# Optimization experiments

Hardware: AMD Instinct MI355X
Metric: run time of the kernel (lower is better)

The kernel has to match this reference:

```python
import jax, jax.numpy as jnp
import numpy as np

N = 50000        # nodes
E = 800000       # edges
F_IN = 32        # float features (x also carries 1 trailing cell-id column)
CELL_DIM = 16
NUM_CELLS = 854
C = 64           # out_channels
H0, H1 = 2, 1    # heads schedule for num_layers=2 -> [2, 1]
D_IN = F_IN + CELL_DIM  # 48, GAT input dim after cell embedding concat
NEG_SLOPE = 0.2  # PyG GATConv default negative_slope


def setup_inputs() -> dict:
    key = jax.random.key(0)
    ks = jax.random.split(key, 14)
    base = jax.random.normal(ks[0], (N, F_IN), jnp.float32)
    cell_ids = jax.random.randint(ks[1], (N,), 0, NUM_CELLS)
    x = jnp.concatenate([base, cell_ids.astype(jnp.float32)[:, None]], axis=1)
    edge_index = jax.random.randint(ks[2], (2, E), 0, N, dtype=jnp.int32)
    s = lambda f: 1.0 / np.sqrt(f)
    emb = jax.random.normal(ks[3], (NUM_CELLS, CELL_DIM), jnp.float32)
    W0 = jax.random.normal(ks[4], (D_IN, H0 * C), jnp.float32) * s(D_IN)
    a_src0 = jax.random.normal(ks[5], (H0, C), jnp.float32) * s(C)
    a_dst0 = jax.random.normal(ks[6], (H0, C), jnp.float32) * s(C)
    b0 = jnp.zeros((C,), jnp.float32)
    ln_g = jnp.ones((C,), jnp.float32)
    ln_b = jnp.zeros((C,), jnp.float32)
    W1 = jax.random.normal(ks[7], (C, H1 * C), jnp.float32) * s(C)
    a_src1 = jax.random.normal(ks[8], (H1, C), jnp.float32) * s(C)
    a_dst1 = jax.random.normal(ks[9], (H1, C), jnp.float32) * s(C)
    b1 = jnp.zeros((C,), jnp.float32)
    return {"x": x, "edge_index": edge_index, "emb": emb,
            "W0": W0, "a_src0": a_src0, "a_dst0": a_dst0, "b0": b0,
            "ln_g": ln_g, "ln_b": ln_b,
            "W1": W1, "a_src1": a_src1, "a_dst1": a_dst1, "b1": b1}


def gat_layer(h_in, src, dst, W, a_src, a_dst, b, heads):
    # h_in: [N, D]; src/dst: [E'] (self-loops already appended)
    h = (h_in @ W).reshape(N, heads, C)                 # [N, H, C]
    alpha_s = jnp.einsum('nhc,hc->nh', h, a_src)        # [N, H]
    alpha_d = jnp.einsum('nhc,hc->nh', h, a_dst)
    e = jax.nn.leaky_relu(alpha_s[src] + alpha_d[dst], NEG_SLOPE)  # [E', H]
    # segment softmax over incoming edges of each dst node
    m = jax.ops.segment_max(e, dst, num_segments=N)     # [N, H]
    ex = jnp.exp(e - m[dst])
    denom = jax.ops.segment_sum(ex, dst, num_segments=N)
    alpha = ex / denom[dst]                             # [E', H]
    msg = h[src] * alpha[:, :, None]                    # [E', H, C]
    out = jax.ops.segment_sum(msg, dst, num_segments=N) # [N, H, C]
    return out.mean(axis=1) + b                         # concat=False -> mean over heads


def layer_norm(x, g, b):
    mu = x.mean(-1, keepdims=True)
    var = ((x - mu) ** 2).mean(-1, keepdims=True)
    return (x - mu) * jax.lax.rsqrt(var + 1e-5) * g + b


def reference(x, edge_index, emb, W0, a_src0, a_dst0, b0, ln_g, ln_b,
              W1, a_src1, a_dst1, b1):
    base = x[:, :-1]
    cell_ids = x[:, -1].astype(jnp.int32)
    h = jnp.concatenate([base, emb[cell_ids]], axis=1)  # [N, 48]
    # add self-loops (PyG GATConv default add_self_loops=True)
    loop = jnp.arange(N, dtype=edge_index.dtype)
    src = jnp.concatenate([edge_index[0], loop])
    dst = jnp.concatenate([edge_index[1], loop])
    h = gat_layer(h, src, dst, W0, a_src0, a_dst0, b0, H0)
    h = jax.nn.elu(layer_norm(h, ln_g, ln_b))           # dropout is identity at eval
    h = gat_layer(h, src, dst, W1, a_src1, a_dst1, b1, H1)
    return h
```

## Files before the change

### kernel.cpp

```cpp
#include <hip/hip_runtime.h>
#include <hip/hip_bf16.h>

#define N_NODES 50000
#define N_EDGES 800000
#define E_TOT 850000
#define F_IN 32
#define CELL_DIM 16
#define D_IN 48
#define X_STRIDE 33
#define NUM_CELLS 854
#define NEG_SLOPE 0.2f
#define SCAN_BLOCKS 49
#define NODE0_BLOCKS 512

typedef unsigned int uint;
typedef unsigned short ushort;

static __device__ __forceinline__ uint f2b(float f) {
  uint x = __float_as_uint(f);
  return (x + 0x7fffu + ((x >> 16) & 1u)) >> 16;
}
static __device__ __forceinline__ float b2f_lo(uint w) { return __uint_as_float(w << 16); }
static __device__ __forceinline__ float b2f_hi(uint w) { return __uint_as_float(w & 0xffff0000u); }
static __device__ __forceinline__ float lrelu(float e) { return e > 0.f ? e : NEG_SLOPE * e; }


__global__ __launch_bounds__(256) void k_hist(const int* __restrict__ ei, int* __restrict__ deg) {
  int e = blockIdx.x * 256 + threadIdx.x;
  if (e < N_EDGES) atomicAdd(&deg[ei[N_EDGES + e]], 1);
}

__global__ __launch_bounds__(1024) void k_scan1(const int* __restrict__ deg, int* __restrict__ off,
                                                int* __restrict__ bsum) {
  __shared__ int ws[16];
  int tid = threadIdx.x;
  int lane = tid & 63, wid = tid >> 6;
  int i = blockIdx.x * 1024 + tid;
  int v = (i < N_NODES) ? deg[i] + 1 : 0;
  int sc = v;
#pragma unroll
  for (int o = 1; o < 64; o <<= 1) {
    int t = __shfl_up(sc, o, 64);
    if (lane >= o) sc += t;
  }
  if (lane == 63) ws[wid] = sc;
  __syncthreads();
  if (tid < 16) {
    int w = ws[tid];
    int s = w;
#pragma unroll
    for (int o = 1; o < 16; o <<= 1) {
      int t = __shfl_up(s, o, 64);
      if (tid >= o) s += t;
    }
    ws[tid] = s - w;
  }
  __syncthreads();
  int excl = sc - v + ws[wid];
  if (i < N_NODES) off[i] = excl;
  if (tid == 1023) bsum[blockIdx.x] = excl + v;
}

__global__ __launch_bounds__(1024) void k_scan23(int* __restrict__ off, int* __restrict__ ofs,
                                                 const int* __restrict__ bsum) {
  __shared__ int carry_s;
  int tid = threadIdx.x;
  if (tid < 64) {
    int v = (tid < SCAN_BLOCKS) ? bsum[tid] : 0;
    int s = v;
#pragma unroll
    for (int o = 1; o < 64; o <<= 1) {
      int t = __shfl_up(s, o, 64);
      if (tid >= o) s += t;
    }
    if (tid == (int)blockIdx.x) carry_s = s - v;
  }
  __syncthreads();
  int carry = carry_s;
  int i = blockIdx.x * 1024 + tid;
  if (i < N_NODES) {
    int v = off[i] + carry;
    off[i] = v;
    ofs[i] = v;
  }
  if (i == 0) off[N_NODES] = E_TOT;
}

__global__ __launch_bounds__(256) void k_scatter(const int* __restrict__ ei, int* __restrict__ ofs,
                                                 const int* __restrict__ off,
                                                 const float2* __restrict__ as0v,
                                                 const float2* __restrict__ ad0v,
                                                 uint2* __restrict__ ew) {
  int t = blockIdx.x * 256 + threadIdx.x;
  if (t < N_EDGES) {
    int s = ei[t], d = ei[N_EDGES + t];
    float2 a_s = as0v[s], a_d = ad0v[d];
    float w0 = __expf(lrelu(a_s.x + a_d.x));
    float w1 = __expf(lrelu(a_s.y + a_d.y));
    int p = atomicAdd(&ofs[d], 1);
    ew[p] = make_uint2((uint)s, f2b(w0) | (f2b(w1) << 16));
  } else if (t < N_EDGES + N_NODES) {
    int n = t - N_EDGES;
    int slot = off[n + 1] - 1;
    float2 a_s = as0v[n], a_d = ad0v[n];
    float w0 = __expf(lrelu(a_s.x + a_d.x));
    float w1 = __expf(lrelu(a_s.y + a_d.y));
    ew[slot] = make_uint2((uint)n, f2b(w0) | (f2b(w1) << 16));
  }
}


__global__ __launch_bounds__(256, 4) void k_node0(const float* __restrict__ x,
                                                  const float* __restrict__ emb,
                                                  const float* __restrict__ W0,
                                                  const float* __restrict__ asrc,
                                                  const float* __restrict__ adst,
                                                  uint* __restrict__ h0p,
                                                  float2* __restrict__ as0,
                                                  float2* __restrict__ ad0) {
  __shared__ float hin_s[4][4][48];
  int tid = threadIdx.x;
  int lane = tid & 63, wid = tid >> 6;
  float2 w0r[D_IN];
#pragma unroll
  for (int k = 0; k < D_IN; ++k)
    w0r[k] = make_float2(W0[k * 128 + lane], W0[k * 128 + 64 + lane]);
  float a_s0 = asrc[lane], a_s1 = asrc[64 + lane];
  float a_d0 = adst[lane], a_d1 = adst[64 + lane];

  int gw = blockIdx.x * 4 + wid;
  for (int g = gw; g < N_NODES / 4; g += NODE0_BLOCKS * 4) {
    int nb = g * 4;
#pragma unroll
    for (int j = 0; j < 4; ++j) {
      int n = nb + j;
      float t = 0.f;
      if (lane < 33) t = x[n * X_STRIDE + lane];
      int cid = (int)__shfl(t, 32, 64);
      cid = cid < 0 ? 0 : (cid >= NUM_CELLS ? NUM_CELLS - 1 : cid);
      if (lane >= 32 && lane < 48) t = emb[cid * CELL_DIM + (lane - 32)];
      if (lane < 48) hin_s[wid][j][lane] = t;
    }
#pragma unroll
    for (int j = 0; j < 4; ++j) {
      int n = nb + j;
      const float4* hp = (const float4*)hin_s[wid][j];
      float acc0 = 0.f, acc1 = 0.f;
#pragma unroll
      for (int k4 = 0; k4 < 12; ++k4) {
        float4 h = hp[k4];
        acc0 = fmaf(h.x, w0r[4 * k4 + 0].x, acc0); acc1 = fmaf(h.x, w0r[4 * k4 + 0].y, acc1);
        acc0 = fmaf(h.y, w0r[4 * k4 + 1].x, acc0); acc1 = fmaf(h.y, w0r[4 * k4 + 1].y, acc1);
        acc0 = fmaf(h.z, w0r[4 * k4 + 2].x, acc0); acc1 = fmaf(h.z, w0r[4 * k4 + 2].y, acc1);
        acc0 = fmaf(h.w, w0r[4 * k4 + 3].x, acc0); acc1 = fmaf(h.w, w0r[4 * k4 + 3].y, acc1);
      }
      h0p[n * 64 + lane] = f2b(acc0) | (f2b(acc1) << 16);
      float sa0 = acc0 * a_s0, sa1 = acc1 * a_s1;
      float sd0 = acc0 * a_d0, sd1 = acc1 * a_d1;
#pragma unroll
      for (int o = 32; o >= 1; o >>= 1) {
        sa0 += __shfl_xor(sa0, o, 64);
        sa1 += __shfl_xor(sa1, o, 64);
        sd0 += __shfl_xor(sd0, o, 64);
        sd1 += __shfl_xor(sd1, o, 64);
      }
      if (lane == 0) {
        as0[n] = make_float2(sa0, sa1);
        ad0[n] = make_float2(sd0, sd1);
      }
    }
  }
}


__global__ __launch_bounds__(256) void k_agg0(const int* __restrict__ off,
                                              const uint2* __restrict__ ew,
                                              const uint* __restrict__ h0p,
                                              const float* __restrict__ b0,
                                              const float* __restrict__ lng,
                                              const float* __restrict__ lnb,
                                              const float* __restrict__ W1,
                                              const float* __restrict__ asrc1,
                                              const float* __restrict__ adst1,
                                              ushort* __restrict__ h1b,
                                              float* __restrict__ as1, float* __restrict__ ad1) {
  int n = blockIdx.x * 4 + (threadIdx.x >> 6);
  int lane = threadIdx.x & 63;
  float acc0 = 0.f, acc1 = 0.f, den0 = 0.f, den1 = 0.f;
  int i0 = off[n], i1 = off[n + 1];
  int i = i0;
  for (; i + 7 < i1; i += 8) {
    uint2 r[8];
    uint h[8];
#pragma unroll
    for (int j = 0; j < 8; ++j) r[j] = ew[i + j];
#pragma unroll
    for (int j = 0; j < 8; ++j) h[j] = h0p[r[j].x * 64 + lane];
#pragma unroll
    for (int j = 0; j < 8; ++j) {
      float w;
      w = b2f_lo(r[j].y); acc0 += w * b2f_lo(h[j]); den0 += w;
      w = b2f_hi(r[j].y); acc1 += w * b2f_hi(h[j]); den1 += w;
    }
  }
  for (; i + 3 < i1; i += 4) {
    uint2 r[4];
    uint h[4];
#pragma unroll
    for (int j = 0; j < 4; ++j) r[j] = ew[i + j];
#pragma unroll
    for (int j = 0; j < 4; ++j) h[j] = h0p[r[j].x * 64 + lane];
#pragma unroll
    for (int j = 0; j < 4; ++j) {
      float w;
      w = b2f_lo(r[j].y); acc0 += w * b2f_lo(h[j]); den0 += w;
      w = b2f_hi(r[j].y); acc1 += w * b2f_hi(h[j]); den1 += w;
    }
  }
  for (; i < i1; ++i) {
    uint2 r = ew[i];
    uint h = h0p[r.x * 64 + lane];
    float w;
    w = b2f_lo(r.y); acc0 += w * b2f_lo(h); den0 += w;
    w = b2f_hi(r.y); acc1 += w * b2f_hi(h); den1 += w;
  }
  float v = 0.5f * (acc0 / den0 + acc1 / den1) + b0[lane];
  float mu = v;
#pragma unroll
  for (int o = 32; o >= 1; o >>= 1) mu += __shfl_xor(mu, o, 64);
  mu *= (1.0f / 64.0f);
  float d = v - mu;
  float vr = d * d;
#pragma unroll
  for (int o = 32; o >= 1; o >>= 1) vr += __shfl_xor(vr, o, 64);
  vr *= (1.0f / 64.0f);
  float y = d * rsqrtf(vr + 1e-5f) * lng[lane] + lnb[lane];
  y = y > 0.f ? y : expm1f(y);
  float h1v = 0.f;
#pragma unroll
  for (int k = 0; k < 64; ++k) {
    float yk = __shfl(y, k, 64);
    h1v += yk * W1[k * 64 + lane];
  }
  h1b[n * 64 + lane] = (ushort)f2b(h1v);
  float sa = h1v * asrc1[lane];
  float sdv = h1v * adst1[lane];
#pragma unroll
  for (int o = 32; o >= 1; o >>= 1) {
    sa += __shfl_xor(sa, o, 64);
    sdv += __shfl_xor(sdv, o, 64);
  }
  if (lane == 0) {
    as1[n] = sa;
    ad1[n] = sdv;
  }
}


__global__ __launch_bounds__(256) void k_agg1(const int* __restrict__ off,
                                              const uint2* __restrict__ ew,
                                              const ushort* __restrict__ h1b,
                                              const float* __restrict__ as1,
                                              const float* __restrict__ ad1,
                                              const float* __restrict__ b1,
                                              float* __restrict__ out) {
  int n = blockIdx.x * 4 + (threadIdx.x >> 6);
  int lane = threadIdx.x & 63;
  float adv = ad1[n];
  float acc = 0.f, den = 0.f;
  int i0 = off[n], i1 = off[n + 1];
  int i = i0;
  for (; i + 7 < i1; i += 8) {
    uint s[8];
    float a[8];
    uint h[8];
#pragma unroll
    for (int j = 0; j < 8; ++j) s[j] = ew[i + j].x;
#pragma unroll
    for (int j = 0; j < 8; ++j) a[j] = as1[s[j]];
#pragma unroll
    for (int j = 0; j < 8; ++j) h[j] = h1b[s[j] * 64 + lane];
#pragma unroll
    for (int j = 0; j < 8; ++j) {
      float w = __expf(lrelu(a[j] + adv));
      acc += w * __uint_as_float(h[j] << 16);
      den += w;
    }
  }
  for (; i + 3 < i1; i += 4) {
    uint s[4];
    float a[4];
    uint h[4];
#pragma unroll
    for (int j = 0; j < 4; ++j) s[j] = ew[i + j].x;
#pragma unroll
    for (int j = 0; j < 4; ++j) a[j] = as1[s[j]];
#pragma unroll
    for (int j = 0; j < 4; ++j) h[j] = h1b[s[j] * 64 + lane];
#pragma unroll
    for (int j = 0; j < 4; ++j) {
      float w = __expf(lrelu(a[j] + adv));
      acc += w * __uint_as_float(h[j] << 16);
      den += w;
    }
  }
  for (; i < i1; ++i) {
    uint s = ew[i].x;
    float w = __expf(lrelu(as1[s] + adv));
    acc += w * __uint_as_float((uint)h1b[s * 64 + lane] << 16);
    den += w;
  }
  out[n * 64 + lane] = acc / den + b1[lane];
}


extern "C" void kernel_launch(void* const* d_in, const int* in_sizes, int n_in,
                              void* d_out, int out_size, void* d_ws, size_t ws_size,
                              hipStream_t stream) {
  const float* x    = (const float*)d_in[0];
  const int*   ei   = (const int*)d_in[1];
  const float* emb  = (const float*)d_in[2];
  const float* W0   = (const float*)d_in[3];
  const float* as0w = (const float*)d_in[4];
  const float* ad0w = (const float*)d_in[5];
  const float* b0   = (const float*)d_in[6];
  const float* lng  = (const float*)d_in[7];
  const float* lnb  = (const float*)d_in[8];
  const float* W1   = (const float*)d_in[9];
  const float* as1w = (const float*)d_in[10];
  const float* ad1w = (const float*)d_in[11];
  const float* b1   = (const float*)d_in[12];
  float* out = (float*)d_out;

  uint2* ew  = (uint2*)d_ws;
  float* as0 = (float*)(ew + E_TOT);
  float* ad0 = as0 + N_NODES * 2;
  float* as1 = ad0 + N_NODES * 2;
  float* ad1 = as1 + N_NODES;
  uint* h0p = (uint*)(ad1 + N_NODES);
  ushort* h1b = (ushort*)(h0p + N_NODES * 64);
  int* deg  = (int*)(h1b + N_NODES * 64);
  int* off  = deg + N_NODES;
  int* ofs  = off + N_NODES + 1;
  int* bsum = ofs + N_NODES;

  hipMemsetAsync(deg, 0, N_NODES * sizeof(int), stream);
  k_node0<<<NODE0_BLOCKS, 256, 0, stream>>>(x, emb, W0, as0w, ad0w, h0p, (float2*)as0,
                                            (float2*)ad0);
  k_hist<<<(N_EDGES + 255) / 256, 256, 0, stream>>>(ei, deg);
  k_scan1<<<SCAN_BLOCKS, 1024, 0, stream>>>(deg, off, bsum);
  k_scan23<<<SCAN_BLOCKS, 1024, 0, stream>>>(off, ofs, bsum);
  k_scatter<<<(N_EDGES + N_NODES + 255) / 256, 256, 0, stream>>>(ei, ofs, off, (const float2*)as0,
                                                                 (const float2*)ad0, ew);
  k_agg0<<<N_NODES / 4, 256, 0, stream>>>(off, ew, h0p, b0, lng, lnb, W1, as1w, ad1w,
                                          h1b, as1, ad1);
  k_agg1<<<N_NODES / 4, 256, 0, stream>>>(off, ew, h1b, as1, ad1, b1, out);
}
```

Measured before the change: 295.0 us.

## Split wavefront across multiple edges with 16-byte gathers and LDS reduction

In both aggregation kernels, each wavefront now processes several edges at once: lane groups each take one edge and load 4 or 8 packed features per lane with a 16-byte vector load, instead of every lane loading 4 or 2 bytes per edge. Partial sums are then combined across lane groups through shared memory. The aim is fewer, wider gather instructions per edge and more edges in flight, which should help a latency-bound gather. The cost is LDS traffic and shared-memory use per block. The cross-lane reduction also has no explicit barrier; it relies on the writing and reading lanes sitting in the same wavefront.

Result: no change. 296.1 us (+0.4%).

```diff
diff --git a/kernel.cpp b/kernel.cpp
--- a/kernel.cpp
+++ b/kernel.cpp
@@ -184,47 +184,54 @@
                                               const float* __restrict__ adst1,
                                               ushort* __restrict__ h1b,
                                               float* __restrict__ as1, float* __restrict__ ad1) {
-  int n = blockIdx.x * 4 + (threadIdx.x >> 6);
+  __shared__ float2 red[4][4][64];
+  __shared__ float2 dred[4][4];
+  int wid = threadIdx.x >> 6;
   int lane = threadIdx.x & 63;
-  float acc0 = 0.f, acc1 = 0.f, den0 = 0.f, den1 = 0.f;
+  int g = lane >> 4;
+  int q = lane & 15;
+  int n = blockIdx.x * 4 + wid;
   int i0 = off[n], i1 = off[n + 1];
+  float a00 = 0.f, a01 = 0.f, a02 = 0.f, a03 = 0.f;
+  float a10 = 0.f, a11 = 0.f, a12 = 0.f, a13 = 0.f;
+  float den0 = 0.f, den1 = 0.f;
   int i = i0;
-  for (; i + 7 < i1; i += 8) {
-    uint2 r[8];
-    uint h[8];
-#pragma unroll
-    for (int j = 0; j < 8; ++j) r[j] = ew[i + j];
-#pragma unroll
-    for (int j = 0; j < 8; ++j) h[j] = h0p[r[j].x * 64 + lane];
-#pragma unroll
-    for (int j = 0; j < 8; ++j) {
-      float w;
-      w = b2f_lo(r[j].y); acc0 += w * b2f_lo(h[j]); den0 += w;
-      w = b2f_hi(r[j].y); acc1 += w * b2f_hi(h[j]); den1 += w;
-    }
-  }
   for (; i + 3 < i1; i += 4) {
-    uint2 r[4];
-    uint h[4];
-#pragma unroll
-    for (int j = 0; j < 4; ++j) r[j] = ew[i + j];
-#pragma unroll
-    for (int j = 0; j < 4; ++j) h[j] = h0p[r[j].x * 64 + lane];
-#pragma unroll
-    for (int j = 0; j < 4; ++j) {
-      float w;
-      w = b2f_lo(r[j].y); acc0 += w * b2f_lo(h[j]); den0 += w;
-      w = b2f_hi(r[j].y); acc1 += w * b2f_hi(h[j]); den1 += w;
-    }
-  }
-  for (; i < i1; ++i) {
-    uint2 r = ew[i];
-    uint h = h0p[r.x * 64 + lane];
-    float w;
-    w = b2f_lo(r.y); acc0 += w * b2f_lo(h); den0 += w;
-    w = b2f_hi(r.y); acc1 += w * b2f_hi(h); den1 += w;
-  }
-  float v = 0.5f * (acc0 / den0 + acc1 / den1) + b0[lane];
+    uint2 r = ew[i + g];
+    uint4 hv = *(const uint4*)(h0p + (size_t)r.x * 64 + q * 4);
+    float w0 = b2f_lo(r.y), w1 = b2f_hi(r.y);
+    a00 += w0 * b2f_lo(hv.x); a10 += w1 * b2f_hi(hv.x);
+    a01 += w0 * b2f_lo(hv.y); a11 += w1 * b2f_hi(hv.y);
+    a02 += w0 * b2f_lo(hv.z); a12 += w1 * b2f_hi(hv.z);
+    a03 += w0 * b2f_lo(hv.w); a13 += w1 * b2f_hi(hv.w);
+    den0 += w0; den1 += w1;
+  }
+  int rem = i1 - i;
+  if (g < rem) {
+    uint2 r = ew[i + g];
+    uint4 hv = *(const uint4*)(h0p + (size_t)r.x * 64 + q * 4);
+    float w0 = b2f_lo(r.y), w1 = b2f_hi(r.y);
+    a00 += w0 * b2f_lo(hv.x); a10 += w1 * b2f_hi(hv.x);
+    a01 += w0 * b2f_lo(hv.y); a11 += w1 * b2f_hi(hv.y);
+    a02 += w0 * b2f_lo(hv.z); a12 += w1 * b2f_hi(hv.z);
+    a03 += w0 * b2f_lo(hv.w); a13 += w1 * b2f_hi(hv.w);
+    den0 += w0; den1 += w1;
+  }
+  red[wid][g][4 * q + 0] = make_float2(a00, a10);
+  red[wid][g][4 * q + 1] = make_float2(a01, a11);
+  red[wid][g][4 * q + 2] = make_float2(a02, a12);
+  red[wid][g][4 * q + 3] = make_float2(a03, a13);
+  if (q == 0) dred[wid][g] = make_float2(den0, den1);
+  float acc0 = 0.f, acc1 = 0.f;
+  float d0 = 0.f, d1 = 0.f;
+#pragma unroll
+  for (int gg = 0; gg < 4; ++gg) {
+    float2 p = red[wid][gg][lane];
+    acc0 += p.x; acc1 += p.y;
+    float2 dd = dred[wid][gg];
+    d0 += dd.x; d1 += dd.y;
+  }
+  float v = 0.5f * (acc0 / d0 + acc1 / d1) + b0[lane];
   float mu = v;
 #pragma unroll
   for (int o = 32; o >= 1; o >>= 1) mu += __shfl_xor(mu, o, 64);
@@ -264,53 +271,55 @@
                                               const float* __restrict__ ad1,
                                               const float* __restrict__ b1,
                                               float* __restrict__ out) {
-  int n = blockIdx.x * 4 + (threadIdx.x >> 6);
+  __shared__ float red[4][8][64];
+  __shared__ float dred[4][8];
+  int wid = threadIdx.x >> 6;
   int lane = threadIdx.x & 63;
+  int g = lane >> 3;
+  int q = lane & 7;
+  int n = blockIdx.x * 4 + wid;
   float adv = ad1[n];
-  float acc = 0.f, den = 0.f;
   int i0 = off[n], i1 = off[n + 1];
+  float a0 = 0.f, a1 = 0.f, a2 = 0.f, a3 = 0.f, a4 = 0.f, a5 = 0.f, a6 = 0.f, a7 = 0.f;
+  float den = 0.f;
   int i = i0;
   for (; i + 7 < i1; i += 8) {
-    uint s[8];
-    float a[8];
-    uint h[8];
-#pragma unroll
-    for (int j = 0; j < 8; ++j) s[j] = ew[i + j].x;
-#pragma unroll
-    for (int j = 0; j < 8; ++j) a[j] = as1[s[j]];
-#pragma unroll
-    for (int j = 0; j < 8; ++j) h[j] = h1b[s[j] * 64 + lane];
-#pragma unroll
-    for (int j = 0; j < 8; ++j) {
-      float w = __expf(lrelu(a[j] + adv));
-      acc += w * __uint_as_float(h[j] << 16);
-      den += w;
-    }
-  }
-  for (; i + 3 < i1; i += 4) {
-    uint s[4];
-    float a[4];
-    uint h[4];
-#pragma unroll
-    for (int j = 0; j < 4; ++j) s[j] = ew[i + j].x;
-#pragma unroll
-    for (int j = 0; j < 4; ++j) a[j] = as1[s[j]];
-#pragma unroll
-    for (int j = 0; j < 4; ++j) h[j] = h1b[s[j] * 64 + lane];
-#pragma unroll
-    for (int j = 0; j < 4; ++j) {
-      float w = __expf(lrelu(a[j] + adv));
-      acc += w * __uint_as_float(h[j] << 16);
-      den += w;
-    }
-  }
-  for (; i < i1; ++i) {
-    uint s = ew[i].x;
+    uint s = ew[i + g].x;
     float w = __expf(lrelu(as1[s] + adv));
-    acc += w * __uint_as_float((uint)h1b[s * 64 + lane] << 16);
+    uint4 hv = *(const uint4*)(h1b + (size_t)s * 64 + q * 8);
+    a0 += w * b2f_lo(hv.x); a1 += w * b2f_hi(hv.x);
+    a2 += w * b2f_lo(hv.y); a3 += w * b2f_hi(hv.y);
+    a4 += w * b2f_lo(hv.z); a5 += w * b2f_hi(hv.z);
+    a6 += w * b2f_lo(hv.w); a7 += w * b2f_hi(hv.w);
     den += w;
   }
-  out[n * 64 + lane] = acc / den + b1[lane];
+  int rem = i1 - i;
+  if (g < rem) {
+    uint s = ew[i + g].x;
+    float w = __expf(lrelu(as1[s] + adv));
+    uint4 hv = *(const uint4*)(h1b + (size_t)s * 64 + q * 8);
+    a0 += w * b2f_lo(hv.x); a1 += w * b2f_hi(hv.x);
+    a2 += w * b2f_lo(hv.y); a3 += w * b2f_hi(hv.y);
+    a4 += w * b2f_lo(hv.z); a5 += w * b2f_hi(hv.z);
+    a6 += w * b2f_lo(hv.w); a7 += w * b2f_hi(hv.w);
+    den += w;
+  }
+  red[wid][g][8 * q + 0] = a0;
+  red[wid][g][8 * q + 1] = a1;
+  red[wid][g][8 * q + 2] = a2;
+  red[wid][g][8 * q + 3] = a3;
+  red[wid][g][8 * q + 4] = a4;
+  red[wid][g][8 * q + 5] = a5;
+  red[wid][g][8 * q + 6] = a6;
+  red[wid][g][8 * q + 7] = a7;
+  if (q == 0) dred[wid][g] = den;
+  float acc = 0.f, dtot = 0.f;
+#pragma unroll
+  for (int gg = 0; gg < 8; ++gg) {
+    acc += red[wid][gg][lane];
+    dtot += dred[wid][gg];
+  }
+  out[n * 64 + lane] = acc / dtot + b1[lane];
 }
 
 
```

## Merge node transform with degree histogram; cooperative edge-list loads in aggregation

Applied to the files above, without the earlier changes.

Combines the node feature transform and the edge in-degree histogram into one launch: the first blocks do the transform and the rest do the histogram atomics, so the two run concurrently and one launch is saved. In both aggregation kernels each wavefront now loads up to 64 edge records at once, one per lane, and broadcasts them by shuffle instead of every lane reading the same records. In layer 1 the per-edge attention exp is computed once per edge rather than in every lane. Edges beyond 64 per node fall back to a serial loop, and the shuffle broadcasts add per-edge ALU work.

Result: slower. 304.7 us (+3.3%).

```diff
diff --git a/kernel.cpp b/kernel.cpp
--- a/kernel.cpp
+++ b/kernel.cpp
@@ -12,6 +12,7 @@
 #define NEG_SLOPE 0.2f
 #define SCAN_BLOCKS 49
 #define NODE0_BLOCKS 512
+#define HIST_BLOCKS 3125
 
 typedef unsigned int uint;
 typedef unsigned short ushort;
@@ -25,10 +26,75 @@
 static __device__ __forceinline__ float lrelu(float e) { return e > 0.f ? e : NEG_SLOPE * e; }
 
 
-__global__ __launch_bounds__(256) void k_hist(const int* __restrict__ ei, int* __restrict__ deg) {
-  int e = blockIdx.x * 256 + threadIdx.x;
-  if (e < N_EDGES) atomicAdd(&deg[ei[N_EDGES + e]], 1);
-}
+__global__ __launch_bounds__(256, 4) void k_node0h(const float* __restrict__ x,
+                                                   const float* __restrict__ emb,
+                                                   const float* __restrict__ W0,
+                                                   const float* __restrict__ asrc,
+                                                   const float* __restrict__ adst,
+                                                   const int* __restrict__ ei,
+                                                   uint* __restrict__ h0p,
+                                                   float2* __restrict__ as0,
+                                                   float2* __restrict__ ad0,
+                                                   int* __restrict__ deg) {
+  int tid = threadIdx.x;
+  if (blockIdx.x >= NODE0_BLOCKS) {
+    int e = (blockIdx.x - NODE0_BLOCKS) * 256 + tid;
+    if (e < N_EDGES) atomicAdd(&deg[ei[N_EDGES + e]], 1);
+    return;
+  }
+  __shared__ float hin_s[4][4][48];
+  int lane = tid & 63, wid = tid >> 6;
+  float2 w0r[D_IN];
+#pragma unroll
+  for (int k = 0; k < D_IN; ++k)
+    w0r[k] = make_float2(W0[k * 128 + lane], W0[k * 128 + 64 + lane]);
+  float a_s0 = asrc[lane], a_s1 = asrc[64 + lane];
+  float a_d0 = adst[lane], a_d1 = adst[64 + lane];
+
+  int gw = blockIdx.x * 4 + wid;
+  for (int g = gw; g < N_NODES / 4; g += NODE0_BLOCKS * 4) {
+    int nb = g * 4;
+#pragma unroll
+    for (int j = 0; j < 4; ++j) {
+      int n = nb + j;
+      float t = 0.f;
+      if (lane < 33) t = x[n * X_STRIDE + lane];
+      int cid = (int)__shfl(t, 32, 64);
+      cid = cid < 0 ? 0 : (cid >= NUM_CELLS ? NUM_CELLS - 1 : cid);
+      if (lane >= 32 && lane < 48) t = emb[cid * CELL_DIM + (lane - 32)];
+      if (lane < 48) hin_s[wid][j][lane] = t;
+    }
+#pragma unroll
+    for (int j = 0; j < 4; ++j) {
+      int n = nb + j;
+      const float4* hp = (const float4*)hin_s[wid][j];
+      float acc0 = 0.f, acc1 = 0.f;
+#pragma unroll
+      for (int k4 = 0; k4 < 12; ++k4) {
+        float4 h = hp[k4];
+        acc0 = fmaf(h.x, w0r[4 * k4 + 0].x, acc0); acc1 = fmaf(h.x, w0r[4 * k4 + 0].y, acc1);
+        acc0 = fmaf(h.y, w0r[4 * k4 + 1].x, acc0); acc1 = fmaf(h.y, w0r[4 * k4 + 1].y, acc1);
+        acc0 = fmaf(h.z, w0r[4 * k4 + 2].x, acc0); acc1 = fmaf(h.z, w0r[4 * k4 + 2].y, acc1);
+        acc0 = fmaf(h.w, w0r[4 * k4 + 3].x, acc0); acc1 = fmaf(h.w, w0r[4 * k4 + 3].y, acc1);
+      }
+      h0p[n * 64 + lane] = f2b(acc0) | (f2b(acc1) << 16);
+      float sa0 = acc0 * a_s0, sa1 = acc1 * a_s1;
+      float sd0 = acc0 * a_d0, sd1 = acc1 * a_d1;
+#pragma unroll
+      for (int o = 32; o >= 1; o >>= 1) {
+        sa0 += __shfl_xor(sa0, o, 64);
+        sa1 += __shfl_xor(sa1, o, 64);
+        sd0 += __shfl_xor(sd0, o, 64);
+        sd1 += __shfl_xor(sd1, o, 64);
+      }
+      if (lane == 0) {
+        as0[n] = make_float2(sa0, sa1);
+        ad0[n] = make_float2(sd0, sd1);
+      }
+    }
+  }
+}
+
 
 __global__ __launch_bounds__(1024) void k_scan1(const int* __restrict__ deg, int* __restrict__ off,
                                                 int* __restrict__ bsum) {
@@ -110,69 +176,6 @@
 }
 
 
-__global__ __launch_bounds__(256, 4) void k_node0(const float* __restrict__ x,
-                                                  const float* __restrict__ emb,
-                                                  const float* __restrict__ W0,
-                                                  const float* __restrict__ asrc,
-                                                  const float* __restrict__ adst,
-                                                  uint* __restrict__ h0p,
-                                                  float2* __restrict__ as0,
-                                                  float2* __restrict__ ad0) {
-  __shared__ float hin_s[4][4][48];
-  int tid = threadIdx.x;
-  int lane = tid & 63, wid = tid >> 6;
-  float2 w0r[D_IN];
-#pragma unroll
-  for (int k = 0; k < D_IN; ++k)
-    w0r[k] = make_float2(W0[k * 128 + lane], W0[k * 128 + 64 + lane]);
-  float a_s0 = asrc[lane], a_s1 = asrc[64 + lane];
-  float a_d0 = adst[lane], a_d1 = adst[64 + lane];
-
-  int gw = blockIdx.x * 4 + wid;
-  for (int g = gw; g < N_NODES / 4; g += NODE0_BLOCKS * 4) {
-    int nb = g * 4;
-#pragma unroll
-    for (int j = 0; j < 4; ++j) {
-      int n = nb + j;
-      float t = 0.f;
-      if (lane < 33) t = x[n * X_STRIDE + lane];
-      int cid = (int)__shfl(t, 32, 64);
-      cid = cid < 0 ? 0 : (cid >= NUM_CELLS ? NUM_CELLS - 1 : cid);
-      if (lane >= 32 && lane < 48) t = emb[cid * CELL_DIM + (lane - 32)];
-      if (lane < 48) hin_s[wid][j][lane] = t;
-    }
-#pragma unroll
-    for (int j = 0; j < 4; ++j) {
-      int n = nb + j;
-      const float4* hp = (const float4*)hin_s[wid][j];
-      float acc0 = 0.f, acc1 = 0.f;
-#pragma unroll
-      for (int k4 = 0; k4 < 12; ++k4) {
-        float4 h = hp[k4];
-        acc0 = fmaf(h.x, w0r[4 * k4 + 0].x, acc0); acc1 = fmaf(h.x, w0r[4 * k4 + 0].y, acc1);
-        acc0 = fmaf(h.y, w0r[4 * k4 + 1].x, acc0); acc1 = fmaf(h.y, w0r[4 * k4 + 1].y, acc1);
-        acc0 = fmaf(h.z, w0r[4 * k4 + 2].x, acc0); acc1 = fmaf(h.z, w0r[4 * k4 + 2].y, acc1);
-        acc0 = fmaf(h.w, w0r[4 * k4 + 3].x, acc0); acc1 = fmaf(h.w, w0r[4 * k4 + 3].y, acc1);
-      }
-      h0p[n * 64 + lane] = f2b(acc0) | (f2b(acc1) << 16);
-      float sa0 = acc0 * a_s0, sa1 = acc1 * a_s1;
-      float sd0 = acc0 * a_d0, sd1 = acc1 * a_d1;
-#pragma unroll
-      for (int o = 32; o >= 1; o >>= 1) {
-        sa0 += __shfl_xor(sa0, o, 64);
-        sa1 += __shfl_xor(sa1, o, 64);
-        sd0 += __shfl_xor(sd0, o, 64);
-        sd1 += __shfl_xor(sd1, o, 64);
-      }
-      if (lane == 0) {
-        as0[n] = make_float2(sa0, sa1);
-        ad0[n] = make_float2(sd0, sd1);
-      }
-    }
-  }
-}
-
-
 __global__ __launch_bounds__(256) void k_agg0(const int* __restrict__ off,
                                               const uint2* __restrict__ ew,
                                               const uint* __restrict__ h0p,
@@ -186,38 +189,45 @@
                                               float* __restrict__ as1, float* __restrict__ ad1) {
   int n = blockIdx.x * 4 + (threadIdx.x >> 6);
   int lane = threadIdx.x & 63;
+  int i0 = off[n], i1 = off[n + 1];
+  int cnt = i1 - i0;
+  int cr = cnt < 64 ? cnt : 64;
+  uint rx = 0, ry = 0;
+  if (lane < cr) {
+    uint2 t = ew[i0 + lane];
+    rx = t.x;
+    ry = t.y;
+  }
   float acc0 = 0.f, acc1 = 0.f, den0 = 0.f, den1 = 0.f;
-  int i0 = off[n], i1 = off[n + 1];
-  int i = i0;
-  for (; i + 7 < i1; i += 8) {
-    uint2 r[8];
-    uint h[8];
-#pragma unroll
-    for (int j = 0; j < 8; ++j) r[j] = ew[i + j];
-#pragma unroll
-    for (int j = 0; j < 8; ++j) h[j] = h0p[r[j].x * 64 + lane];
-#pragma unroll
-    for (int j = 0; j < 8; ++j) {
-      float w;
-      w = b2f_lo(r[j].y); acc0 += w * b2f_lo(h[j]); den0 += w;
-      w = b2f_hi(r[j].y); acc1 += w * b2f_hi(h[j]); den1 += w;
-    }
-  }
-  for (; i + 3 < i1; i += 4) {
-    uint2 r[4];
-    uint h[4];
-#pragma unroll
-    for (int j = 0; j < 4; ++j) r[j] = ew[i + j];
-#pragma unroll
-    for (int j = 0; j < 4; ++j) h[j] = h0p[r[j].x * 64 + lane];
-#pragma unroll
-    for (int j = 0; j < 4; ++j) {
-      float w;
-      w = b2f_lo(r[j].y); acc0 += w * b2f_lo(h[j]); den0 += w;
-      w = b2f_hi(r[j].y); acc1 += w * b2f_hi(h[j]); den1 += w;
-    }
-  }
-  for (; i < i1; ++i) {
+  int j = 0;
+  for (; j + 3 < cr; j += 4) {
+    uint s0 = __shfl(rx, j, 64), s1 = __shfl(rx, j + 1, 64);
+    uint s2 = __shfl(rx, j + 2, 64), s3 = __shfl(rx, j + 3, 64);
+    uint w0 = __shfl(ry, j, 64), w1 = __shfl(ry, j + 1, 64);
+    uint w2 = __shfl(ry, j + 2, 64), w3 = __shfl(ry, j + 3, 64);
+    uint h0 = h0p[s0 * 64 + lane];
+    uint h1 = h0p[s1 * 64 + lane];
+    uint h2 = h0p[s2 * 64 + lane];
+    uint h3 = h0p[s3 * 64 + lane];
+    float w;
+    w = b2f_lo(w0); acc0 += w * b2f_lo(h0); den0 += w;
+    w = b2f_hi(w0); acc1 += w * b2f_hi(h0); den1 += w;
+    w = b2f_lo(w1); acc0 += w * b2f_lo(h1); den0 += w;
+    w = b2f_hi(w1); acc1 += w * b2f_hi(h1); den1 += w;
+    w = b2f_lo(w2); acc0 += w * b2f_lo(h2); den0 += w;
+    w = b2f_hi(w2); acc1 += w * b2f_hi(h2); den1 += w;
+    w = b2f_lo(w3); acc0 += w * b2f_lo(h3); den0 += w;
+    w = b2f_hi(w3); acc1 += w * b2f_hi(h3); den1 += w;
+  }
+  for (; j < cr; ++j) {
+    uint s = __shfl(rx, j, 64);
+    uint wp = __shfl(ry, j, 64);
+    uint h = h0p[s * 64 + lane];
+    float w;
+    w = b2f_lo(wp); acc0 += w * b2f_lo(h); den0 += w;
+    w = b2f_hi(wp); acc1 += w * b2f_hi(h); den1 += w;
+  }
+  for (int i = i0 + 64; i < i1; ++i) {
     uint2 r = ew[i];
     uint h = h0p[r.x * 64 + lane];
     float w;
@@ -267,44 +277,39 @@
   int n = blockIdx.x * 4 + (threadIdx.x >> 6);
   int lane = threadIdx.x & 63;
   float adv = ad1[n];
+  int i0 = off[n], i1 = off[n + 1];
+  int cnt = i1 - i0;
+  int cr = cnt < 64 ? cnt : 64;
+  uint rx = 0;
+  float rw = 0.f;
+  if (lane < cr) {
+    rx = ew[i0 + lane].x;
+    rw = __expf(lrelu(as1[rx] + adv));
+  }
   float acc = 0.f, den = 0.f;
-  int i0 = off[n], i1 = off[n + 1];
-  int i = i0;
-  for (; i + 7 < i1; i += 8) {
-    uint s[8];
-    float a[8];
-    uint h[8];
-#pragma unroll
-    for (int j = 0; j < 8; ++j) s[j] = ew[i + j].x;
-#pragma unroll
-    for (int j = 0; j < 8; ++j) a[j] = as1[s[j]];
-#pragma unroll
-    for (int j = 0; j < 8; ++j) h[j] = h1b[s[j] * 64 + lane];
-#pragma unroll
-    for (int j = 0; j < 8; ++j) {
-      float w = __expf(lrelu(a[j] + adv));
-      acc += w * __uint_as_float(h[j] << 16);
-      den += w;
-    }
-  }
-  for (; i + 3 < i1; i += 4) {
-    uint s[4];
-    float a[4];
-    uint h[4];
-#pragma unroll
-    for (int j = 0; j < 4; ++j) s[j] = ew[i + j].x;
-#pragma unroll
-    for (int j = 0; j < 4; ++j) a[j] = as1[s[j]];
-#pragma unroll
-    for (int j = 0; j < 4; ++j) h[j] = h1b[s[j] * 64 + lane];
-#pragma unroll
-    for (int j = 0; j < 4; ++j) {
-      float w = __expf(lrelu(a[j] + adv));
-      acc += w * __uint_as_float(h[j] << 16);
-      den += w;
-    }
-  }
-  for (; i < i1; ++i) {
+  int j = 0;
+  for (; j + 3 < cr; j += 4) {
+    uint s0 = __shfl(rx, j, 64), s1 = __shfl(rx, j + 1, 64);
+    uint s2 = __shfl(rx, j + 2, 64), s3 = __shfl(rx, j + 3, 64);
+    float w0 = __shfl(rw, j, 64), w1 = __shfl(rw, j + 1, 64);
+    float w2 = __shfl(rw, j + 2, 64), w3 = __shfl(rw, j + 3, 64);
+    uint h0 = h1b[s0 * 64 + lane];
+    uint h1 = h1b[s1 * 64 + lane];
+    uint h2 = h1b[s2 * 64 + lane];
+    uint h3 = h1b[s3 * 64 + lane];
+    acc += w0 * __uint_as_float(h0 << 16); den += w0;
+    acc += w1 * __uint_as_float(h1 << 16); den += w1;
+    acc += w2 * __uint_as_float(h2 << 16); den += w2;
+    acc += w3 * __uint_as_float(h3 << 16); den += w3;
+  }
+  for (; j < cr; ++j) {
+    uint s = __shfl(rx, j, 64);
+    float w = __shfl(rw, j, 64);
+    uint h = h1b[s * 64 + lane];
+    acc += w * __uint_as_float(h << 16);
+    den += w;
+  }
+  for (int i = i0 + 64; i < i1; ++i) {
     uint s = ew[i].x;
     float w = __expf(lrelu(as1[s] + adv));
     acc += w * __uint_as_float((uint)h1b[s * 64 + lane] << 16);
@@ -345,9 +350,8 @@
   int* bsum = ofs + N_NODES;
 
   hipMemsetAsync(deg, 0, N_NODES * sizeof(int), stream);
-  k_node0<<<NODE0_BLOCKS, 256, 0, stream>>>(x, emb, W0, as0w, ad0w, h0p, (float2*)as0,
-                                            (float2*)ad0);
-  k_hist<<<(N_EDGES + 255) / 256, 256, 0, stream>>>(ei, deg);
+  k_node0h<<<NODE0_BLOCKS + HIST_BLOCKS, 256, 0, stream>>>(x, emb, W0, as0w, ad0w, ei, h0p,
+                                                           (float2*)as0, (float2*)ad0, deg);
   k_scan1<<<SCAN_BLOCKS, 1024, 0, stream>>>(deg, off, bsum);
   k_scan23<<<SCAN_BLOCKS, 1024, 0, stream>>>(off, ofs, bsum);
   k_scatter<<<(N_EDGES + N_NODES + 255) / 256, 256, 0, stream>>>(ei, ofs, off, (const float2*)as0,
```
